# Optimization experiments

Hardware: AMD Instinct MI355X
Metric: run time of the kernel (lower is better)

The kernel has to match this reference:

```python
import jax, jax.numpy as jnp
from jax import lax
import numpy as np

VOCAB, E, H, T = 8000, 300, 75, 6  # H = hidden_dim//2 per direction
B, S = 256, 512
START, STOP = 4, 5
NEG = -10000.0


def setup_inputs() -> dict:
    key = jax.random.key(0)
    ks = jax.random.split(key, 16)
    sc = 0.1  # keep activations in sane range
    trans = jax.random.normal(ks[14], (T, T), jnp.float32)
    trans = trans.at[START, :].set(NEG).at[:, STOP].set(NEG)
    return {
        "sentence": jax.random.randint(ks[0], (B, S), 0, VOCAB),
        "tags": jax.random.randint(ks[1], (B, S), 0, 4),  # only B/I/E/S gold tags
        "embedding": jax.random.normal(ks[2], (VOCAB, E), jnp.float32),
        "w_ih_f": sc * jax.random.normal(ks[3], (4 * H, E), jnp.float32),
        "w_hh_f": sc * jax.random.normal(ks[4], (4 * H, H), jnp.float32),
        "b_ih_f": sc * jax.random.normal(ks[5], (4 * H,), jnp.float32),
        "b_hh_f": sc * jax.random.normal(ks[6], (4 * H,), jnp.float32),
        "w_ih_b": sc * jax.random.normal(ks[7], (4 * H, E), jnp.float32),
        "w_hh_b": sc * jax.random.normal(ks[8], (4 * H, H), jnp.float32),
        "b_ih_b": sc * jax.random.normal(ks[9], (4 * H,), jnp.float32),
        "b_hh_b": sc * jax.random.normal(ks[10], (4 * H,), jnp.float32),
        "h0": jax.random.normal(ks[11], (2, B, H), jnp.float32),
        "c0": jax.random.normal(ks[12], (2, B, H), jnp.float32),
        "w_out": sc * jax.random.normal(ks[13], (T, 2 * H), jnp.float32),
        "b_out": sc * jax.random.normal(ks[15], (T,), jnp.float32),
        "transitions": trans,
    }


def _lstm_dir(xg, w_hh, h0, c0, reverse):
    # xg: [S, B, 4H] precomputed input gates; PyTorch gate order i, f, g, o
    def step(carry, g):
        h, c = carry
        gates = g + h @ w_hh.T
        i, f, gg, o = jnp.split(gates, 4, axis=-1)
        c = jax.nn.sigmoid(f) * c + jax.nn.sigmoid(i) * jnp.tanh(gg)
        h = jax.nn.sigmoid(o) * jnp.tanh(c)
        return (h, c), h

    _, hs = lax.scan(step, (h0, c0), xg, reverse=reverse)
    return hs  # [S, B, H]


def reference(sentence, tags, embedding, w_ih_f, w_hh_f, b_ih_f, b_hh_f,
              w_ih_b, w_hh_b, b_ih_b, b_hh_b, h0, c0, w_out, b_out, transitions):
    # --- BiLSTM features ---
    embeds = embedding[sentence].transpose(1, 0, 2)  # [S, B, E]
    xg_f = embeds @ w_ih_f.T + (b_ih_f + b_hh_f)
    xg_b = embeds @ w_ih_b.T + (b_ih_b + b_hh_b)
    hf = _lstm_dir(xg_f, w_hh_f, h0[0], c0[0], reverse=False)
    hb = _lstm_dir(xg_b, w_hh_b, h0[1], c0[1], reverse=True)
    lstm_out = jnp.concatenate([hf, hb], axis=-1)  # [S, B, 2H]
    feats = lstm_out @ w_out.T + b_out  # [S, B, T]

    # --- CRF forward algorithm (log partition) ---
    alpha0 = jnp.full((feats.shape[1], T), NEG, feats.dtype).at[:, START].set(0.0)

    def crf_step(alpha, feat):
        # alpha_new[b, j] = logsumexp_i(alpha[b, i] + trans[j, i] + feat[b, j])
        alpha = jax.nn.logsumexp(
            alpha[:, None, :] + transitions[None, :, :] + feat[:, :, None], axis=2)
        return alpha, None

    alpha, _ = lax.scan(crf_step, alpha0, feats)
    forward_score = jax.nn.logsumexp(alpha + transitions[STOP][None, :], axis=1)  # [B]

    # --- gold path score ---
    tags_ext = jnp.concatenate(
        [jnp.full((tags.shape[0], 1), START, tags.dtype), tags], axis=1)  # [B, S+1]
    trans_sc = transitions[tags_ext[:, 1:], tags_ext[:, :-1]].sum(axis=1)  # [B]
    feats_bt = feats.transpose(1, 0, 2)  # [B, S, T]
    emit_sc = jnp.take_along_axis(feats_bt, tags[:, :, None], axis=2)[..., 0].sum(axis=1)
    gold_score = trans_sc + emit_sc + transitions[STOP, tags[:, -1]]

    return forward_score - gold_score  # [B] per-sentence CRF NLL
```

## Files before the change

kernel.cpp:

```cpp
#include <hip/hip_runtime.h>
#include <stdint.h>

#define VOCABN 8000
#define EE     300
#define HH     75
#define G4     300
#define TT     6
#define BB     256
#define SS     512
#define STARTT 4
#define STOPT  5
#define NEGV   (-10000.0f)
#define NCH    16
#define CHL    32

typedef __fp16 fp16x2 __attribute__((ext_vector_type(2)));
typedef __fp16 f16x4 __attribute__((ext_vector_type(4)));
typedef __fp16 f16x8 __attribute__((ext_vector_type(8)));
typedef float f32x4 __attribute__((ext_vector_type(4)));
typedef unsigned int u32;
typedef unsigned short u16;

__device__ __forceinline__ float sigf(float x){
  return __builtin_amdgcn_rcpf(1.0f + __expf(-x));
}
__device__ __forceinline__ float tanhf_(float x){
  return __builtin_fmaf(__builtin_amdgcn_rcpf(1.0f + __expf(-2.0f * x)), 2.0f, -1.0f);
}
__device__ __forceinline__ float pk2(float a, float b){
  fp16x2 r = __builtin_amdgcn_cvt_pkrtz(a, b);
  return __builtin_bit_cast(float, r);
}
__device__ __forceinline__ float dot2pk(float a, float b, float c){
  asm("v_dot2_f32_f16 %0, %1, %2, %0" : "+v"(c) : "v"(a), "v"(b));
  return c;
}
__device__ __forceinline__ void sync_lds(){
  __builtin_amdgcn_sched_barrier(0);
  asm volatile("s_waitcnt lgkmcnt(0)" ::: "memory");
  __builtin_amdgcn_s_barrier();
  __builtin_amdgcn_sched_barrier(0);
}

#define LDSR 20
__global__ __launch_bounds__(256) void k_gemm(
    const float* __restrict__ emb, const float* __restrict__ w_ih_f,
    const float* __restrict__ w_ih_b,
    const float* __restrict__ b_ih_f, const float* __restrict__ b_hh_f,
    const float* __restrict__ b_ih_b, const float* __restrict__ b_hh_b,
    __fp16* __restrict__ vxg){
  __shared__ alignas(16) float a_sh[128 * LDSR];
  __shared__ alignas(16) float b_sh[64 * LDSR];
  __shared__ float bias_sh[64];
  const int bx = blockIdx.x;
  const int dir = bx / (63 * 5);
  const int rem = bx % (63 * 5);
  const int vt = rem / 5, gt = rem % 5;
  const int v0 = vt * 128, g0 = gt * 64;
  const int tid = threadIdx.x;
  const float* wdir = dir ? w_ih_b : w_ih_f;

  if (tid < 64){
    int g = g0 + tid;
    float bi = 0.f;
    if (g < G4){
      int gs = (g & 3) * 75 + (g >> 2);
      bi = dir ? (b_ih_b[gs] + b_hh_b[gs]) : (b_ih_f[gs] + b_hh_f[gs]);
    }
    bias_sh[tid] = bi;
  }

  float acc[8][4];
  #pragma unroll
  for (int i = 0; i < 8; ++i)
    #pragma unroll
    for (int j = 0; j < 4; ++j) acc[i][j] = 0.f;

  const int tx = tid & 15, ty = tid >> 4;
  const int la_r = tid >> 1, la_h = (tid & 1) * 8;
  const int lb_r = tid >> 2, lb_h = (tid & 3) * 4;

  const int va = v0 + la_r;
  const float* arow = emb + (size_t)(va < VOCABN ? va : 0) * EE;
  const int gb = g0 + lb_r;
  const int gsrc = (gb & 3) * 75 + (gb >> 2);
  const float* brow = wdir + (size_t)(gb < G4 ? gsrc : 0) * EE;
  const float4 z4 = {0.f, 0.f, 0.f, 0.f};

  for (int kk = 0; kk < 19; ++kk){
    const int e0 = kk * 16;
    float4 av0 = *(const float4*)&arow[e0 + la_h];
    float4 av1 = (e0 + la_h + 7 < EE) ? *(const float4*)&arow[e0 + la_h + 4] : z4;
    float4 bv  = (e0 + lb_h + 3 < EE) ? *(const float4*)&brow[e0 + lb_h]     : z4;
    __syncthreads();
    *(float4*)&a_sh[la_r * LDSR + la_h]     = av0;
    *(float4*)&a_sh[la_r * LDSR + la_h + 4] = av1;
    *(float4*)&b_sh[lb_r * LDSR + lb_h]     = bv;
    __syncthreads();
    #pragma unroll
    for (int e4 = 0; e4 < 4; ++e4){
      float4 bq[4], aq[8];
      #pragma unroll
      for (int j = 0; j < 4; ++j) bq[j] = *(const float4*)&b_sh[(tx + 16 * j) * LDSR + e4 * 4];
      #pragma unroll
      for (int i = 0; i < 8; ++i) aq[i] = *(const float4*)&a_sh[(ty + 16 * i) * LDSR + e4 * 4];
      #pragma unroll
      for (int i = 0; i < 8; ++i)
        #pragma unroll
        for (int j = 0; j < 4; ++j)
          acc[i][j] += aq[i].x * bq[j].x + aq[i].y * bq[j].y
                     + aq[i].z * bq[j].z + aq[i].w * bq[j].w;
    }
  }

  const size_t obase = (size_t)dir * VOCABN * G4;
  #pragma unroll
  for (int i = 0; i < 8; ++i){
    int v = v0 + ty + 16 * i;
    if (v < VOCABN){
      #pragma unroll
      for (int j = 0; j < 4; ++j){
        int g = g0 + tx + 16 * j;
        if (g < G4)
          vxg[obase + (size_t)v * G4 + g] = (__fp16)(acc[i][j] + bias_sh[tx + 16 * j]);
      }
    }
  }
}

__global__ __launch_bounds__(640) void k_lstm(
    const int* __restrict__ sentence, const __fp16* __restrict__ vxg,
    const float* __restrict__ w_hh_f, const float* __restrict__ w_hh_b,
    const float* __restrict__ h0, const float* __restrict__ c0,
    const float* __restrict__ w_out, const float* __restrict__ b_out,
    float* __restrict__ featsF, float* __restrict__ featsB){
  __shared__ u16 tok_sh[SS * 16];
  __shared__ alignas(16) __fp16 hfrag[2][12 * 16 * 8];
  const int bx = blockIdx.x;
  const int dir = bx >> 4, group = bx & 15;
  const int t = threadIdx.x;
  const int w = t >> 6, lane = t & 63;
  const int bb = lane & 15, q = lane >> 4;
  const int T0 = 2 * w, T1 = 2 * w + 1;
  const int rbA = 16 * T0 + 4 * q, rbB = 16 * T1 + 4 * q;
  const int hA = rbA >> 2, hB = rbB >> 2;
  const int bglob = group * 16 + bb;
  const int wiA = w * 128 + bb * 8 + q;
  const int wiB = w * 128 + bb * 8 + 4 + q;

  for (int i = t; i < 2 * 12 * 16 * 4; i += 640) ((u32*)hfrag)[i] = 0;
  for (int i = t; i < 16 * SS; i += 640){
    int bq = i >> 9, s = i & 511;
    tok_sh[s * 16 + ((bq + s) & 15)] =
        (u16)sentence[(size_t)(group * 16 + bq) * SS + s];
  }
  __syncthreads();

  const float* whh = dir ? w_hh_b : w_hh_f;
  f16x8 a00, a01, a02, a10, a11, a12;
  #define BUILD_A(dst, T, c) { \
    int m = 16 * (T) + bb; int kb = 32 * (c) + 8 * q; \
    _Pragma("unroll") \
    for (int j = 0; j < 8; ++j){ \
      int kk = kb + j; float wv = 0.f; \
      if (kk < HH){ \
        if (m < 300) wv = whh[((m & 3) * 75 + (m >> 2)) * HH + kk]; \
        else if (m < 306) wv = w_out[(m - 300) * (2 * HH) + dir * HH + kk]; \
      } \
      dst[j] = (__fp16)wv; } }
  BUILD_A(a00, T0, 0) BUILD_A(a01, T0, 1) BUILD_A(a02, T0, 2)
  BUILD_A(a10, T1, 0) BUILD_A(a11, T1, 1) BUILD_A(a12, T1, 2)

  float cA = 0.f, cB = 0.f;
  if (hA < HH){
    cA = c0[((size_t)dir * BB + bglob) * HH + hA];
    hfrag[0][wiA] = (__fp16)h0[((size_t)dir * BB + bglob) * HH + hA];
  }
  if (hB < HH){
    cB = c0[((size_t)dir * BB + bglob) * HH + hB];
    hfrag[0][wiB] = (__fp16)h0[((size_t)dir * BB + bglob) * HH + hB];
  }
  const float bo0 = dir ? 0.f : b_out[0], bo1 = dir ? 0.f : b_out[1];
  const float bo2 = dir ? 0.f : b_out[2], bo3 = dir ? 0.f : b_out[3];
  const float bo4 = dir ? 0.f : b_out[4], bo5 = dir ? 0.f : b_out[5];
  __syncthreads();

  const __fp16* vx = vxg + (size_t)dir * VOCABN * G4;
  float* feats = dir ? featsB : featsF;
  const f16x4 zh4 = {(__fp16)0.f, (__fp16)0.f, (__fp16)0.f, (__fp16)0.f};

#define LOADPAIR(d0, d1, kstep) { \
    if ((kstep) < SS){ \
      int sr_ = dir ? (SS - 1 - (kstep)) : (kstep); \
      int tk_ = tok_sh[sr_ * 16 + ((bb + sr_) & 15)]; \
      const __fp16* base_ = vx + (size_t)tk_ * G4; \
      d0 = (hA < HH) ? *(const f16x4*)(base_ + rbA) : zh4; \
      d1 = (hB < HH) ? *(const f16x4*)(base_ + rbB) : zh4; \
    } else { d0 = zh4; d1 = zh4; } }

  f16x4 cur0, cur1, nx0, nx1, p0, p1;
  LOADPAIR(cur0, cur1, 0)
  LOADPAIR(nx0, nx1, 1)

  for (int k = 0; k <= SS; ++k){
    const __fp16* hq = hfrag[k & 1];
    f16x8 b0 = *(const f16x8*)&hq[(0 * 64 + lane) * 8];
    f16x8 b1 = *(const f16x8*)&hq[(1 * 64 + lane) * 8];
    f16x8 b2 = *(const f16x8*)&hq[(2 * 64 + lane) * 8];

    LOADPAIR(p0, p1, k + 2)

    f32x4 acc0 = {0.f, 0.f, 0.f, 0.f}, acc1 = {0.f, 0.f, 0.f, 0.f};
    asm("v_mfma_f32_16x16x32_f16 %0, %1, %2, %0" : "+v"(acc0) : "a"(a00), "v"(b0));
    asm("v_mfma_f32_16x16x32_f16 %0, %1, %2, %0" : "+v"(acc1) : "a"(a10), "v"(b0));
    asm("v_mfma_f32_16x16x32_f16 %0, %1, %2, %0" : "+v"(acc0) : "a"(a01), "v"(b1));
    asm("v_mfma_f32_16x16x32_f16 %0, %1, %2, %0" : "+v"(acc1) : "a"(a11), "v"(b1));
    asm("v_mfma_f32_16x16x32_f16 %0, %1, %2, %0" : "+v"(acc0) : "a"(a02), "v"(b2));
    asm("v_mfma_f32_16x16x32_f16 %0, %1, %2, %0" : "+v"(acc1) : "a"(a12), "v"(b2));

    __fp16* hw = hfrag[(k & 1) ^ 1];
    if (k < SS){
      if (hA < HH){
        float gi = acc0.x + (float)cur0.x, gf = acc0.y + (float)cur0.y;
        float gg = acc0.z + (float)cur0.z, go = acc0.w + (float)cur0.w;
        cA = sigf(gf) * cA + sigf(gi) * tanhf_(gg);
        hw[wiA] = (__fp16)(sigf(go) * tanhf_(cA));
      }
      if (hB < HH){
        float gi = acc1.x + (float)cur1.x, gf = acc1.y + (float)cur1.y;
        float gg = acc1.z + (float)cur1.z, go = acc1.w + (float)cur1.w;
        cB = sigf(gf) * cB + sigf(gi) * tanhf_(gg);
        hw[wiB] = (__fp16)(sigf(go) * tanhf_(cB));
      }
    }
    if (k >= 1){
      if (rbA == 300){
        int ps = dir ? (SS - k) : (k - 1);
        float* fb = feats + ((size_t)ps * BB + bglob) * TT;
        float2 v01 = {acc0.x + (float)cur0.x + bo0, acc0.y + (float)cur0.y + bo1};
        float2 v23 = {acc0.z + (float)cur0.z + bo2, acc0.w + (float)cur0.w + bo3};
        *(float2*)fb = v01;
        *(float2*)(fb + 2) = v23;
      }
      if (rbB == 304){
        int ps = dir ? (SS - k) : (k - 1);
        float* fb = feats + ((size_t)ps * BB + bglob) * TT;
        float2 v45 = {acc1.x + (float)cur1.x + bo4, acc1.y + (float)cur1.y + bo5};
        *(float2*)(fb + 4) = v45;
      }
    }
    cur0 = nx0; cur1 = nx1; nx0 = p0; nx1 = p1;
    sync_lds();
  }
}

#define LOADSTAGE(X0,X1,X2,Y0,Y1,Y2, srow) do{ \
  int _r = (srow); if (_r >= SS) _r = 0; \
  const float2* _pF = (const float2*)(featsF + ((size_t)_r * BB + b) * TT); \
  const float2* _pB = (const float2*)(featsB + ((size_t)_r * BB + b) * TT); \
  X0 = _pF[0]; X1 = _pF[1]; X2 = _pF[2]; \
  Y0 = _pB[0]; Y1 = _pB[1]; Y2 = _pB[2]; }while(0)

#define ASTEP(X0,X1,X2,Y0,Y1,Y2, srow) do{ \
  float F0 = X0.x + Y0.x, F1 = X0.y + Y0.y, F2 = X1.x + Y1.x; \
  float F3 = X1.y + Y1.y, F4 = X2.x + Y2.x, F5 = X2.y + Y2.y; \
  float M = fmaxf(fmaxf(fmaxf(a0,a1),fmaxf(a2,a3)),fmaxf(a4,a5)); \
  float p01 = pk2(__expf(a0-M), __expf(a1-M)); \
  float p23 = pk2(__expf(a2-M), __expf(a3-M)); \
  float p45 = pk2(__expf(a4-M), __expf(a5-M)); \
  float s0 = dot2pk(p45, Tq2,  dot2pk(p23, Tq1,  dot2pk(p01, Tq0,  0.f))); \
  float s1 = dot2pk(p45, Tq5,  dot2pk(p23, Tq4,  dot2pk(p01, Tq3,  0.f))); \
  float s2 = dot2pk(p45, Tq8,  dot2pk(p23, Tq7,  dot2pk(p01, Tq6,  0.f))); \
  float s3 = dot2pk(p45, Tq11, dot2pk(p23, Tq10, dot2pk(p01, Tq9,  0.f))); \
  float s4 = dot2pk(p45, Tq14, dot2pk(p23, Tq13, dot2pk(p01, Tq12, 0.f))); \
  float s5 = dot2pk(p45, Tq17, dot2pk(p23, Tq16, dot2pk(p01, Tq15, 0.f))); \
  a0 = M + __logf(fmaxf(s0, 1e-37f)) + F0;  a1 = M + __logf(fmaxf(s1, 1e-37f)) + F1; \
  a2 = M + __logf(fmaxf(s2, 1e-37f)) + F2;  a3 = M + __logf(fmaxf(s3, 1e-37f)) + F3; \
  a4 = M + __logf(fmaxf(s4, 1e-37f)) + F4;  a5 = M + __logf(fmaxf(s5, 1e-37f)) + F5; \
  LOADSTAGE(X0,X1,X2,Y0,Y1,Y2, (srow) + 2); }while(0)

__global__ __launch_bounds__(256) void k_crf_scan(
    const float* __restrict__ featsF, const float* __restrict__ featsB,
    const float* __restrict__ trans, const int* __restrict__ tags,
    float* __restrict__ crfM, float* __restrict__ pgold){
  __shared__ float tr_sh[36];
  __shared__ u32 etp_sh[18];
  const int tid = threadIdx.x;
  if (tid < 36) tr_sh[tid] = trans[tid];
  if (tid < 18) etp_sh[tid] = __float_as_uint(
      pk2(__expf(trans[2 * tid]), __expf(trans[2 * tid + 1])));
  __syncthreads();
  const int bx = blockIdx.x;

  if (bx < 96){
    const int g = bx * 256 + tid;
    const int s0i = g % 6;
    const int c = (g / 6) % NCH;
    const int b = g / (6 * NCH);
    const int cbase = c * CHL;

    float Tq0=__int_as_float(etp_sh[0]),  Tq1=__int_as_float(etp_sh[1]),
          Tq2=__int_as_float(etp_sh[2]),  Tq3=__int_as_float(etp_sh[3]),
          Tq4=__int_as_float(etp_sh[4]),  Tq5=__int_as_float(etp_sh[5]),
          Tq6=__int_as_float(etp_sh[6]),  Tq7=__int_as_float(etp_sh[7]),
          Tq8=__int_as_float(etp_sh[8]),  Tq9=__int_as_float(etp_sh[9]),
          Tq10=__int_as_float(etp_sh[10]), Tq11=__int_as_float(etp_sh[11]),
          Tq12=__int_as_float(etp_sh[12]), Tq13=__int_as_float(etp_sh[13]),
          Tq14=__int_as_float(etp_sh[14]), Tq15=__int_as_float(etp_sh[15]),
          Tq16=__int_as_float(etp_sh[16]), Tq17=__int_as_float(etp_sh[17]);

    float a0 = (s0i == 0) ? 0.f : NEGV, a1 = (s0i == 1) ? 0.f : NEGV;
    float a2 = (s0i == 2) ? 0.f : NEGV, a3 = (s0i == 3) ? 0.f : NEGV;
    float a4 = (s0i == 4) ? 0.f : NEGV, a5 = (s0i == 5) ? 0.f : NEGV;

    float2 xA0,xA1,xA2,yA0,yA1,yA2, xB0,xB1,xB2,yB0,yB1,yB2;
    LOADSTAGE(xA0,xA1,xA2,yA0,yA1,yA2, cbase + 0);
    LOADSTAGE(xB0,xB1,xB2,yB0,yB1,yB2, cbase + 1);
    for (int s = 0; s < CHL; s += 2){
      ASTEP(xA0,xA1,xA2,yA0,yA1,yA2, cbase + s);
      ASTEP(xB0,xB1,xB2,yB0,yB1,yB2, cbase + s + 1);
    }
    float* mrow = crfM + ((size_t)(b * NCH + c) * 6 + s0i) * 6;
    mrow[0] = a0; mrow[1] = a1; mrow[2] = a2;
    mrow[3] = a3; mrow[4] = a4; mrow[5] = a5;
  } else {
    const int g2 = (bx - 96) * 256 + tid;
    const int b = g2 / NCH;
    const int c = g2 % NCH;
    const int* tg = tags + (size_t)b * SS + c * CHL;
    int prev = (c == 0) ? STARTT : tg[-1];
    float acc = 0.f;
    #pragma unroll 4
    for (int s = 0; s < CHL; ++s){
      int ct = tg[s];
      size_t fo = (size_t)(c * CHL + s) * BB * TT + (size_t)b * TT + ct;
      acc += tr_sh[ct * 6 + prev] + featsF[fo] + featsB[fo];
      prev = ct;
    }
    pgold[b * NCH + c] = acc;
  }
}

__global__ __launch_bounds__(64) void k_crf_comb(
    const float* __restrict__ crfM, const float* __restrict__ pgold,
    const float* __restrict__ trans, const int* __restrict__ tags,
    float* __restrict__ out){
  const int b = blockIdx.x * 64 + threadIdx.x;
  float v0 = NEGV, v1 = NEGV, v2 = NEGV, v3 = NEGV, v4 = 0.f, v5 = NEGV;
  for (int c = 0; c < NCH; ++c){
    const float* mb = crfM + (size_t)(b * NCH + c) * 36;
    float n[6];
    #pragma unroll
    for (int j = 0; j < 6; ++j){
      float t0 = v0 + mb[0 * 6 + j], t1 = v1 + mb[1 * 6 + j];
      float t2 = v2 + mb[2 * 6 + j], t3 = v3 + mb[3 * 6 + j];
      float t4 = v4 + mb[4 * 6 + j], t5 = v5 + mb[5 * 6 + j];
      float m = fmaxf(fmaxf(fmaxf(t0,t1),fmaxf(t2,t3)),fmaxf(t4,t5));
      float s = __expf(t0-m)+__expf(t1-m)+__expf(t2-m)
              + __expf(t3-m)+__expf(t4-m)+__expf(t5-m);
      n[j] = m + __logf(s);
    }
    v0 = n[0]; v1 = n[1]; v2 = n[2]; v3 = n[3]; v4 = n[4]; v5 = n[5];
  }
  float z0 = v0 + trans[30], z1 = v1 + trans[31], z2 = v2 + trans[32];
  float z3 = v3 + trans[33], z4 = v4 + trans[34], z5 = v5 + trans[35];
  float M2 = fmaxf(fmaxf(fmaxf(z0,z1),fmaxf(z2,z3)),fmaxf(z4,z5));
  float ss = __expf(z0-M2)+__expf(z1-M2)+__expf(z2-M2)
           + __expf(z3-M2)+__expf(z4-M2)+__expf(z5-M2);
  float fwd = M2 + __logf(ss);

  float gold = trans[STOPT * 6 + tags[(size_t)b * SS + SS - 1]];
  #pragma unroll
  for (int c = 0; c < NCH; ++c) gold += pgold[b * NCH + c];
  out[b] = fwd - gold;
}

extern "C" void kernel_launch(void* const* d_in, const int* in_sizes, int n_in,
                              void* d_out, int out_size, void* d_ws, size_t ws_size,
                              hipStream_t stream){
  const int*   sentence = (const int*)  d_in[0];
  const int*   tags     = (const int*)  d_in[1];
  const float* emb      = (const float*)d_in[2];
  const float* w_ih_f   = (const float*)d_in[3];
  const float* w_hh_f   = (const float*)d_in[4];
  const float* b_ih_f   = (const float*)d_in[5];
  const float* b_hh_f   = (const float*)d_in[6];
  const float* w_ih_b   = (const float*)d_in[7];
  const float* w_hh_b   = (const float*)d_in[8];
  const float* b_ih_b   = (const float*)d_in[9];
  const float* b_hh_b   = (const float*)d_in[10];
  const float* h0       = (const float*)d_in[11];
  const float* c0       = (const float*)d_in[12];
  const float* w_out    = (const float*)d_in[13];
  const float* b_out    = (const float*)d_in[14];
  const float* trans    = (const float*)d_in[15];
  float* out = (float*)d_out;

  __fp16* vxg  = (__fp16*)d_ws;
  float* featsF = (float*)(vxg + (size_t)2 * VOCABN * G4);
  float* featsB = featsF + (size_t)SS * BB * TT;
  float* crfM   = featsB + (size_t)SS * BB * TT;
  float* pgold  = crfM + (size_t)BB * NCH * 36;

  k_gemm<<<2 * 63 * 5, 256, 0, stream>>>(emb, w_ih_f, w_ih_b,
                                         b_ih_f, b_hh_f, b_ih_b, b_hh_b, vxg);
  k_lstm<<<32, 640, 0, stream>>>(sentence, vxg, w_hh_f, w_hh_b, h0, c0, w_out, b_out,
                                 featsF, featsB);
  k_crf_scan<<<96 + 16, 256, 0, stream>>>(featsF, featsB, trans, tags, crfM, pgold);
  k_crf_comb<<<BB / 64, 64, 0, stream>>>(crfM, pgold, trans, tags, out);
}
```

Measured before the change: 537.2 us.

## Rewrite vocab-gate GEMM with fp16 MFMA 16x16x32 instructions

Replaces the FP32 LDS-tiled SIMT GEMM that precomputes per-vocabulary input gates with an MFMA-based kernel. Each block handles 64 vocab rows across all 300 gate columns; A fragments are converted to fp16 in registers and B fragments are staged in LDS in fp16. This cuts the scalar FMA cost of the table GEMM but adds fp16 rounding on inputs and reloads the weights from global memory for every block.

Measured after the change: 568.5 us. 1.06x slower.

```diff
diff --git a/kernel.cpp b/kernel.cpp
--- a/kernel.cpp
+++ b/kernel.cpp
@@ -42,87 +42,90 @@
   __builtin_amdgcn_sched_barrier(0);
 }
 
-#define LDSR 20
 __global__ __launch_bounds__(256) void k_gemm(
     const float* __restrict__ emb, const float* __restrict__ w_ih_f,
     const float* __restrict__ w_ih_b,
     const float* __restrict__ b_ih_f, const float* __restrict__ b_hh_f,
     const float* __restrict__ b_ih_b, const float* __restrict__ b_hh_b,
     __fp16* __restrict__ vxg){
-  __shared__ alignas(16) float a_sh[128 * LDSR];
-  __shared__ alignas(16) float b_sh[64 * LDSR];
-  __shared__ float bias_sh[64];
+  __shared__ alignas(16) __fp16 bfrag[19 * 64 * 8];
+  __shared__ float bias_sh[304];
   const int bx = blockIdx.x;
-  const int dir = bx / (63 * 5);
-  const int rem = bx % (63 * 5);
-  const int vt = rem / 5, gt = rem % 5;
-  const int v0 = vt * 128, g0 = gt * 64;
+  const int dir = bx / 125;
+  const int vblk = bx % 125;
+  const int v0 = vblk * 64;
   const int tid = threadIdx.x;
+  const int w = tid >> 6, lane = tid & 63;
+  const int bb = lane & 15, q = lane >> 4;
   const float* wdir = dir ? w_ih_b : w_ih_f;
 
-  if (tid < 64){
-    int g = g0 + tid;
+  for (int g = tid; g < 304; g += 256){
     float bi = 0.f;
     if (g < G4){
       int gs = (g & 3) * 75 + (g >> 2);
       bi = dir ? (b_ih_b[gs] + b_hh_b[gs]) : (b_ih_f[gs] + b_hh_f[gs]);
     }
-    bias_sh[tid] = bi;
-  }
-
-  float acc[8][4];
+    bias_sh[g] = bi;
+  }
+
+  f32x4 acc[19];
   #pragma unroll
-  for (int i = 0; i < 8; ++i)
+  for (int t = 0; t < 19; ++t) acc[t] = (f32x4){0.f, 0.f, 0.f, 0.f};
+
+  const float* arow = emb + (size_t)(v0 + 16 * w + bb) * EE;
+
+  for (int c = 0; c < 10; ++c){
+    f16x8 afrag;
+    const int kb = 32 * c + 8 * q;
+    if (c < 9){
+      float4 x0 = *(const float4*)(arow + kb);
+      float4 x1 = *(const float4*)(arow + kb + 4);
+      afrag[0] = (__fp16)x0.x; afrag[1] = (__fp16)x0.y;
+      afrag[2] = (__fp16)x0.z; afrag[3] = (__fp16)x0.w;
+      afrag[4] = (__fp16)x1.x; afrag[5] = (__fp16)x1.y;
+      afrag[6] = (__fp16)x1.z; afrag[7] = (__fp16)x1.w;
+    } else {
+      #pragma unroll
+      for (int j = 0; j < 8; ++j)
+        afrag[j] = (kb + j < EE) ? (__fp16)arow[kb + j] : (__fp16)0.f;
+    }
+
+    for (int g = tid; g < 304; g += 256){
+      int t = g >> 4, col = g & 15;
+      bool valid = g < G4;
+      const float* wrow = wdir + (size_t)(valid ? ((g & 3) * 75 + (g >> 2)) : 0) * EE;
+      #pragma unroll
+      for (int qq = 0; qq < 4; ++qq){
+        f16x8 tmp;
+        #pragma unroll
+        for (int j = 0; j < 8; ++j){
+          int kk = 32 * c + 8 * qq + j;
+          tmp[j] = (valid && kk < EE) ? (__fp16)wrow[kk] : (__fp16)0.f;
+        }
+        *(f16x8*)&bfrag[(t * 64 + qq * 16 + col) * 8] = tmp;
+      }
+    }
+    __syncthreads();
+
     #pragma unroll
-    for (int j = 0; j < 4; ++j) acc[i][j] = 0.f;
-
-  const int tx = tid & 15, ty = tid >> 4;
-  const int la_r = tid >> 1, la_h = (tid & 1) * 8;
-  const int lb_r = tid >> 2, lb_h = (tid & 3) * 4;
-
-  const int va = v0 + la_r;
-  const float* arow = emb + (size_t)(va < VOCABN ? va : 0) * EE;
-  const int gb = g0 + lb_r;
-  const int gsrc = (gb & 3) * 75 + (gb >> 2);
-  const float* brow = wdir + (size_t)(gb < G4 ? gsrc : 0) * EE;
-  const float4 z4 = {0.f, 0.f, 0.f, 0.f};
-
-  for (int kk = 0; kk < 19; ++kk){
-    const int e0 = kk * 16;
-    float4 av0 = *(const float4*)&arow[e0 + la_h];
-    float4 av1 = (e0 + la_h + 7 < EE) ? *(const float4*)&arow[e0 + la_h + 4] : z4;
-    float4 bv  = (e0 + lb_h + 3 < EE) ? *(const float4*)&brow[e0 + lb_h]     : z4;
+    for (int t = 0; t < 19; ++t){
+      f16x8 bf = *(const f16x8*)&bfrag[(t * 64 + lane) * 8];
+      asm("v_mfma_f32_16x16x32_f16 %0, %1, %2, %0"
+          : "+v"(acc[t]) : "v"(afrag), "v"(bf));
+    }
     __syncthreads();
-    *(float4*)&a_sh[la_r * LDSR + la_h]     = av0;
-    *(float4*)&a_sh[la_r * LDSR + la_h + 4] = av1;
-    *(float4*)&b_sh[lb_r * LDSR + lb_h]     = bv;
-    __syncthreads();
-    #pragma unroll
-    for (int e4 = 0; e4 < 4; ++e4){
-      float4 bq[4], aq[8];
-      #pragma unroll
-      for (int j = 0; j < 4; ++j) bq[j] = *(const float4*)&b_sh[(tx + 16 * j) * LDSR + e4 * 4];
-      #pragma unroll
-      for (int i = 0; i < 8; ++i) aq[i] = *(const float4*)&a_sh[(ty + 16 * i) * LDSR + e4 * 4];
-      #pragma unroll
-      for (int i = 0; i < 8; ++i)
-        #pragma unroll
-        for (int j = 0; j < 4; ++j)
-          acc[i][j] += aq[i].x * bq[j].x + aq[i].y * bq[j].y
-                     + aq[i].z * bq[j].z + aq[i].w * bq[j].w;
-    }
   }
 
   const size_t obase = (size_t)dir * VOCABN * G4;
   #pragma unroll
-  for (int i = 0; i < 8; ++i){
-    int v = v0 + ty + 16 * i;
-    if (v < VOCABN){
+  for (int t = 0; t < 19; ++t){
+    int g = 16 * t + bb;
+    if (g < G4){
+      float bi = bias_sh[g];
       #pragma unroll
-      for (int j = 0; j < 4; ++j){
-        int g = g0 + tx + 16 * j;
-        if (g < G4)
-          vxg[obase + (size_t)v * G4 + g] = (__fp16)(acc[i][j] + bias_sh[tx + 16 * j]);
+      for (int r = 0; r < 4; ++r){
+        int v = v0 + 16 * w + 4 * q + r;
+        vxg[obase + (size_t)v * G4 + g] = (__fp16)(acc[t][r] + bi);
       }
     }
   }
@@ -402,8 +405,8 @@
   float* crfM   = featsB + (size_t)SS * BB * TT;
   float* pgold  = crfM + (size_t)BB * NCH * 36;
 
-  k_gemm<<<2 * 63 * 5, 256, 0, stream>>>(emb, w_ih_f, w_ih_b,
-                                         b_ih_f, b_hh_f, b_ih_b, b_hh_b, vxg);
+  k_gemm<<<2 * 125, 256, 0, stream>>>(emb, w_ih_f, w_ih_b,
+                                      b_ih_f, b_hh_f, b_ih_b, b_hh_b, vxg);
   k_lstm<<<32, 640, 0, stream>>>(sentence, vxg, w_hh_f, w_hh_b, h0, c0, w_out, b_out,
                                  featsF, featsB);
   k_crf_scan<<<96 + 16, 256, 0, stream>>>(featsF, featsB, trans, tags, crfM, pgold);
```
